# Kernel tuning notes

Measured on AMD Instinct MI355X. Metric: run time of the kernel, lower is better.

Reference implementation:

```python
import jax, jax.numpy as jnp
import numpy as np

N_NODES = 50000
N_EDGES = 800000
D_IN = 64
D_HID = 64
N_LAYERS = 3


def setup_inputs() -> dict:
    key = jax.random.key(0)
    ks = jax.random.split(key, 3 + 2 * N_LAYERS)
    x = jax.random.normal(ks[0], (N_NODES, D_IN), dtype=jnp.float32)
    edge_index = jax.random.randint(ks[1], (2, N_EDGES), 0, N_NODES, dtype=jnp.int64)
    edge_weight = jax.random.uniform(ks[2], (N_EDGES,), dtype=jnp.float32)
    inp = {"x": x, "edge_index": edge_index, "edge_weight": edge_weight}
    dims = [(D_IN, D_HID)] + [(D_HID, D_HID)] * (N_LAYERS - 1)
    for i, (din, dout) in enumerate(dims):
        # Glorot-style init like PyG GCNConv
        scale = jnp.sqrt(6.0 / (din + dout)).astype(jnp.float32)
        inp[f"W{i}"] = jax.random.uniform(ks[3 + 2 * i], (din, dout), dtype=jnp.float32, minval=-1.0, maxval=1.0) * scale
        inp[f"b{i}"] = jnp.zeros((dout,), dtype=jnp.float32)
    return inp


def _gcn_norm(edge_index, edge_weight, num_nodes, dtype):
    # Add self-loops with weight 1, then symmetric normalization (PyG gcn_norm).
    loop = jnp.arange(num_nodes)
    src = jnp.concatenate([edge_index[0], loop])
    dst = jnp.concatenate([edge_index[1], loop])
    w = jnp.concatenate([edge_weight, jnp.ones((num_nodes,), dtype=dtype)])
    deg = jax.ops.segment_sum(w, dst, num_segments=num_nodes)  # [N]
    dinv = jnp.where(deg > 0, jax.lax.rsqrt(deg), jnp.zeros_like(deg))
    norm = dinv[src] * w * dinv[dst]  # [E+N]
    return src, dst, norm


def reference(x, edge_index, edge_weight, W0, b0, W1, b1, W2, b2):
    N = x.shape[0]
    src, dst, norm = _gcn_norm(edge_index, edge_weight, N, x.dtype)
    for W, b in ((W0, b0), (W1, b1), (W2, b2)):
        h = x @ W                                   # [N, dout] linear first (PyG)
        msg = h[src] * norm[:, None]                # gather + scale per edge
        x = jax.ops.segment_sum(msg, dst, num_segments=N) + b  # scatter-add + bias
        x = jax.nn.relu(x)
    return x
```

## Files before the change

kernel.cpp:

```cpp
#include <hip/hip_runtime.h>

#define NN 50000
#define NE 800000
#define D  64
#define NB 782
#define NBLK 256
#define CHUNK 3125
#define CAP 1536
#define CAPTOT (NB * CAP)

__device__ __forceinline__ float blo(unsigned u) { return __uint_as_float(u << 16); }
__device__ __forceinline__ float bhi(unsigned u) { return __uint_as_float(u & 0xFFFF0000u); }
__device__ __forceinline__ unsigned short f2b(float f) {
    unsigned u = __float_as_uint(f);
    return (unsigned short)((u + 0x7FFFu + ((u >> 16) & 1u)) >> 16);
}

__global__ void k_init(int* __restrict__ cursor) {
    int i = blockIdx.x * blockDim.x + threadIdx.x;
    if (i < NB) cursor[i] = i * CAP;
}

__global__ __launch_bounds__(256) void p12(const int* __restrict__ src,
        const int* __restrict__ dst, const float* __restrict__ w,
        int* __restrict__ cursor, int2* __restrict__ stage) {
    __shared__ unsigned se[CHUNK];
    __shared__ float    sw[CHUNK];
    __shared__ int      lh[NB];
    int t = threadIdx.x;
    for (int i = t; i < NB; i += 256) lh[i] = 0;
    __syncthreads();
    int e0 = blockIdx.x * CHUNK;
    for (int i = t; i < CHUNK; i += 256) {
        int e = e0 + i;
        unsigned d = (unsigned)dst[e];
        unsigned s = (unsigned)src[e];
        float wv = w[e];
        unsigned pk = 0xFFFFFFFFu;
        if (d < NN) {
            pk = (s & 0xFFFFu) | ((d & 63u) << 16) | ((d >> 6) << 22);
            atomicAdd(&lh[d >> 6], 1);
        }
        se[i] = pk;
        sw[i] = wv;
    }
    __syncthreads();
    for (int i = t; i < NB; i += 256) {
        int c = lh[i];
        lh[i] = c ? atomicAdd(&cursor[i], c) : 0;
    }
    __syncthreads();
    for (int i = t; i < CHUNK; i += 256) {
        unsigned pk = se[i];
        if (pk != 0xFFFFFFFFu) {
            int bucket = (int)(pk >> 22);
            int pos = atomicAdd(&lh[bucket], 1);
            if (pos < (bucket + 1) * CAP)
                stage[pos] = make_int2((int)(pk & 0x3FFFFFu), __float_as_int(sw[i]));
        }
    }
}

__global__ __launch_bounds__(256) void p3_sort(const int2* __restrict__ stage,
        const int* __restrict__ cursor, int2* __restrict__ csr,
        int* __restrict__ row_ptr, int* __restrict__ row_deg, float* __restrict__ dinv) {
    __shared__ int   hist[64];
    __shared__ int   cur[64];
    __shared__ float wsum[64];
    int b = blockIdx.x, t = threadIdx.x;
    int g0 = b * CAP, g1 = cursor[b];
    if (t < 64) { hist[t] = 0; wsum[t] = 0.f; }
    __syncthreads();
    for (int j = g0 + t; j < g1; j += 256) {
        int2 pk = stage[j];
        int r = (pk.x >> 16) & 63;
        atomicAdd(&hist[r], 1);
        atomicAdd(&wsum[r], __int_as_float(pk.y));
    }
    __syncthreads();
    if (t == 0) {
        int s = g0;
        for (int r = 0; r < 64; ++r) { cur[r] = s; s += hist[r]; }
    }
    __syncthreads();
    if (t < 64) {
        int n = b * 64 + t;
        if (n < NN) {
            row_ptr[n] = cur[t];
            row_deg[n] = hist[t];
            dinv[n] = rsqrtf(wsum[t] + 1.0f);
        }
    }
    __syncthreads();
    for (int j = g0 + t; j < g1; j += 256) {
        int2 pk = stage[j];
        int r = (pk.x >> 16) & 63;
        int pos = atomicAdd(&cur[r], 1);
        csr[pos] = make_int2(pk.x & 0xFFFF, pk.y);
    }
}

__global__ __launch_bounds__(256) void gemm_pre_kernel(const float* __restrict__ x,
        const float* __restrict__ W, const float* __restrict__ dinv,
        unsigned short* __restrict__ hp) {
    __shared__ float xs[16][64];
    int t = threadIdx.x;
    int base = blockIdx.x * 16;
    for (int idx = t; idx < 16 * 64; idx += 256)
        xs[idx >> 6][idx & 63] = x[(size_t)(base + (idx >> 6)) * 64 + (idx & 63)];
    __syncthreads();
    int col = t & 63, rq = t >> 6;
    float wc[64];
#pragma unroll
    for (int k = 0; k < 64; ++k) wc[k] = W[k * 64 + col];
    float acc0 = 0.f, acc1 = 0.f, acc2 = 0.f, acc3 = 0.f;
#pragma unroll
    for (int k = 0; k < 64; ++k) {
        float wk = wc[k];
        acc0 += xs[rq     ][k] * wk;
        acc1 += xs[rq +  4][k] * wk;
        acc2 += xs[rq +  8][k] * wk;
        acc3 += xs[rq + 12][k] * wk;
    }
    int r = base + rq;
    hp[(size_t)(r     ) * 64 + col] = f2b(dinv[r     ] * acc0);
    hp[(size_t)(r +  4) * 64 + col] = f2b(dinv[r +  4] * acc1);
    hp[(size_t)(r +  8) * 64 + col] = f2b(dinv[r +  8] * acc2);
    hp[(size_t)(r + 12) * 64 + col] = f2b(dinv[r + 12] * acc3);
}

__device__ __forceinline__ float4 gather_row(int n, int fq,
        const int* __restrict__ row_ptr, const int* __restrict__ row_deg,
        const int2* __restrict__ csr, const uint2* __restrict__ hp64) {
    int s0 = row_ptr[n], s1 = s0 + row_deg[n];
    uint2 self = hp64[(size_t)n * 16 + fq];
    float ax = blo(self.x), ay = bhi(self.x), az = blo(self.y), aw = bhi(self.y);
    float bx = 0.f, by = 0.f, bz = 0.f, bw = 0.f;
    for (int base = s0; base < s1; base += 8) {
        uint2 u[8]; float wv[8];
#pragma unroll
        for (int jj = 0; jj < 8; ++jj) {
            int j = base + jj;
            if (j < s1) {
                int2 pk = csr[j];
                wv[jj] = __int_as_float(pk.y);
                u[jj]  = hp64[((size_t)(unsigned)pk.x << 4) + fq];
            } else {
                wv[jj] = 0.f;
                u[jj]  = make_uint2(0u, 0u);
            }
        }
#pragma unroll
        for (int jj = 0; jj < 8; jj += 2) {
            float w0 = wv[jj], w1 = wv[jj + 1];
            ax += w0 * blo(u[jj].x);     ay += w0 * bhi(u[jj].x);
            az += w0 * blo(u[jj].y);     aw += w0 * bhi(u[jj].y);
            bx += w1 * blo(u[jj + 1].x); by += w1 * bhi(u[jj + 1].x);
            bz += w1 * blo(u[jj + 1].y); bw += w1 * bhi(u[jj + 1].y);
        }
    }
    return make_float4(ax + bx, ay + by, az + bz, aw + bw);
}

__global__ __launch_bounds__(256) void fused_kernel(const int* __restrict__ row_ptr,
        const int* __restrict__ row_deg, const int2* __restrict__ csr,
        const float* __restrict__ dinv, const uint2* __restrict__ hp_cur,
        const float* __restrict__ bias, const float* __restrict__ Wn,
        unsigned short* __restrict__ hp_next) {
    __shared__ float ys[16][64];
    int t = threadIdx.x;
    int lane = t & 63, q = lane >> 4, fq = lane & 15;
    int ni = ((t >> 6) << 2) + q;
    int n = blockIdx.x * 16 + ni;
    float4 g = gather_row(n, fq, row_ptr, row_deg, csr, hp_cur);
    float dv = dinv[n];
    float4 bb = ((const float4*)bias)[fq];
    float4 y;
    y.x = fmaxf(dv * g.x + bb.x, 0.f);
    y.y = fmaxf(dv * g.y + bb.y, 0.f);
    y.z = fmaxf(dv * g.z + bb.z, 0.f);
    y.w = fmaxf(dv * g.w + bb.w, 0.f);
    ((float4*)ys[ni])[fq] = y;
    __syncthreads();
    int col = lane, rq = t >> 6;
    float wc[64];
#pragma unroll
    for (int k = 0; k < 64; ++k) wc[k] = Wn[k * 64 + col];
    float a0 = 0.f, a1 = 0.f, a2 = 0.f, a3 = 0.f;
#pragma unroll
    for (int k = 0; k < 64; ++k) {
        float wk = wc[k];
        a0 += ys[rq     ][k] * wk;
        a1 += ys[rq +  4][k] * wk;
        a2 += ys[rq +  8][k] * wk;
        a3 += ys[rq + 12][k] * wk;
    }
    int r = blockIdx.x * 16 + rq;
    hp_next[(size_t)(r     ) * 64 + col] = f2b(dinv[r     ] * a0);
    hp_next[(size_t)(r +  4) * 64 + col] = f2b(dinv[r +  4] * a1);
    hp_next[(size_t)(r +  8) * 64 + col] = f2b(dinv[r +  8] * a2);
    hp_next[(size_t)(r + 12) * 64 + col] = f2b(dinv[r + 12] * a3);
}

__global__ __launch_bounds__(256) void final_kernel(const int* __restrict__ row_ptr,
        const int* __restrict__ row_deg, const int2* __restrict__ csr,
        const float* __restrict__ dinv, const uint2* __restrict__ hp_cur,
        const float* __restrict__ bias, float* __restrict__ out) {
    int t = threadIdx.x;
    int lane = t & 63, q = lane >> 4, fq = lane & 15;
    int n = blockIdx.x * 16 + ((t >> 6) << 2) + q;
    float4 g = gather_row(n, fq, row_ptr, row_deg, csr, hp_cur);
    float dv = dinv[n];
    float4 bb = ((const float4*)bias)[fq];
    float4 r;
    r.x = fmaxf(dv * g.x + bb.x, 0.f);
    r.y = fmaxf(dv * g.y + bb.y, 0.f);
    r.z = fmaxf(dv * g.z + bb.z, 0.f);
    r.w = fmaxf(dv * g.w + bb.w, 0.f);
    ((float4*)out)[(size_t)n * 16 + fq] = r;
}

extern "C" void kernel_launch(void* const* d_in, const int* in_sizes, int n_in,
                              void* d_out, int out_size, void* d_ws, size_t ws_size,
                              hipStream_t stream) {
    const float* x  = (const float*)d_in[0];
    const int*   ei = (const int*)d_in[1];
    const float* ew = (const float*)d_in[2];
    const float* W0 = (const float*)d_in[3];
    const float* b0 = (const float*)d_in[4];
    const float* W1 = (const float*)d_in[5];
    const float* b1 = (const float*)d_in[6];
    const float* W2 = (const float*)d_in[7];
    const float* b2 = (const float*)d_in[8];
    float*       out = (float*)d_out;

    const int* src = ei;
    const int* dst = ei + NE;

    int2*  stage   = (int2*)d_ws;
    int2*  csr     = stage + CAPTOT;
    int*   cursor  = (int*)(csr + CAPTOT);
    int*   row_ptr = cursor + NB;
    int*   row_deg = row_ptr + NN;
    float* dinv    = (float*)(row_deg + NN);
    unsigned short* hpA = (unsigned short*)(dinv + NN);
    unsigned short* hpB = hpA + (size_t)NN * 64;

    k_init<<<1, 1024, 0, stream>>>(cursor);
    p12<<<NBLK, 256, 0, stream>>>(src, dst, ew, cursor, stage);
    p3_sort<<<NB, 256, 0, stream>>>(stage, cursor, csr, row_ptr, row_deg, dinv);

    gemm_pre_kernel<<<NN / 16, 256, 0, stream>>>(x, W0, dinv, hpA);
    fused_kernel<<<NN / 16, 256, 0, stream>>>(row_ptr, row_deg, csr, dinv,
            (const uint2*)hpA, b0, W1, hpB);
    fused_kernel<<<NN / 16, 256, 0, stream>>>(row_ptr, row_deg, csr, dinv,
            (const uint2*)hpB, b1, W2, hpA);
    final_kernel<<<NN / 16, 256, 0, stream>>>(row_ptr, row_deg, csr, dinv,
            (const uint2*)hpA, b2, out);
}
```

Measured before the change: 218.7 us.

## Gather each node with a full wave splitting edges across lanes

The aggregation now assigns one 64-lane wave per node instead of 16 lanes per node. The lanes form 8 edge slots of 8 lanes, and each lane loads 16 bytes of bf16 features. Partial sums are combined with cross-lane xor shuffles, and blocks grow to 1024 threads so that 16 nodes still fit per block. This targets imbalance and serialized latency on high-degree rows and raises memory-level parallelism per edge. The cost is four times as many threads, shuffle reductions, and a dense step where each lane now computes one output rather than four. The hp buffers are also moved earlier in the workspace, likely for alignment of the 16-byte loads.

```diff
diff --git a/kernel.cpp b/kernel.cpp
--- a/kernel.cpp
+++ b/kernel.cpp
@@ -129,95 +129,106 @@
     hp[(size_t)(r + 12) * 64 + col] = f2b(dinv[r + 12] * acc3);
 }
 
-__device__ __forceinline__ float4 gather_row(int n, int fq,
+__device__ __forceinline__ void gather_wave(int n, int slot, int fo,
         const int* __restrict__ row_ptr, const int* __restrict__ row_deg,
-        const int2* __restrict__ csr, const uint2* __restrict__ hp64) {
+        const int2* __restrict__ csr, const uint4* __restrict__ hp4,
+        float acc[8]) {
     int s0 = row_ptr[n], s1 = s0 + row_deg[n];
-    uint2 self = hp64[(size_t)n * 16 + fq];
-    float ax = blo(self.x), ay = bhi(self.x), az = blo(self.y), aw = bhi(self.y);
-    float bx = 0.f, by = 0.f, bz = 0.f, bw = 0.f;
-    for (int base = s0; base < s1; base += 8) {
-        uint2 u[8]; float wv[8];
-#pragma unroll
-        for (int jj = 0; jj < 8; ++jj) {
-            int j = base + jj;
-            if (j < s1) {
-                int2 pk = csr[j];
-                wv[jj] = __int_as_float(pk.y);
-                u[jj]  = hp64[((size_t)(unsigned)pk.x << 4) + fq];
-            } else {
-                wv[jj] = 0.f;
-                u[jj]  = make_uint2(0u, 0u);
-            }
-        }
-#pragma unroll
-        for (int jj = 0; jj < 8; jj += 2) {
-            float w0 = wv[jj], w1 = wv[jj + 1];
-            ax += w0 * blo(u[jj].x);     ay += w0 * bhi(u[jj].x);
-            az += w0 * blo(u[jj].y);     aw += w0 * bhi(u[jj].y);
-            bx += w1 * blo(u[jj + 1].x); by += w1 * bhi(u[jj + 1].x);
-            bz += w1 * blo(u[jj + 1].y); bw += w1 * bhi(u[jj + 1].y);
-        }
-    }
-    return make_float4(ax + bx, ay + by, az + bz, aw + bw);
-}
-
-__global__ __launch_bounds__(256) void fused_kernel(const int* __restrict__ row_ptr,
+    uint4 sv = hp4[(size_t)n * 8 + fo];
+    bool keep = (slot == 0);
+    acc[0] = keep ? blo(sv.x) : 0.f;  acc[1] = keep ? bhi(sv.x) : 0.f;
+    acc[2] = keep ? blo(sv.y) : 0.f;  acc[3] = keep ? bhi(sv.y) : 0.f;
+    acc[4] = keep ? blo(sv.z) : 0.f;  acc[5] = keep ? bhi(sv.z) : 0.f;
+    acc[6] = keep ? blo(sv.w) : 0.f;  acc[7] = keep ? bhi(sv.w) : 0.f;
+    for (int base = s0; base < s1; base += 16) {
+        int j0 = base + slot, j1 = base + 8 + slot;
+        int src0 = 0; float w0 = 0.f;
+        int src1 = 0; float w1 = 0.f;
+        if (j0 < s1) { int2 pk = csr[j0]; src0 = pk.x; w0 = __int_as_float(pk.y); }
+        if (j1 < s1) { int2 pk = csr[j1]; src1 = pk.x; w1 = __int_as_float(pk.y); }
+        uint4 u0 = hp4[(size_t)src0 * 8 + fo];
+        uint4 u1 = hp4[(size_t)src1 * 8 + fo];
+        acc[0] += w0 * blo(u0.x);  acc[1] += w0 * bhi(u0.x);
+        acc[2] += w0 * blo(u0.y);  acc[3] += w0 * bhi(u0.y);
+        acc[4] += w0 * blo(u0.z);  acc[5] += w0 * bhi(u0.z);
+        acc[6] += w0 * blo(u0.w);  acc[7] += w0 * bhi(u0.w);
+        acc[0] += w1 * blo(u1.x);  acc[1] += w1 * bhi(u1.x);
+        acc[2] += w1 * blo(u1.y);  acc[3] += w1 * bhi(u1.y);
+        acc[4] += w1 * blo(u1.z);  acc[5] += w1 * bhi(u1.z);
+        acc[6] += w1 * blo(u1.w);  acc[7] += w1 * bhi(u1.w);
+    }
+#pragma unroll
+    for (int m = 8; m <= 32; m <<= 1) {
+#pragma unroll
+        for (int i = 0; i < 8; ++i) acc[i] += __shfl_xor(acc[i], m, 64);
+    }
+}
+
+__global__ __launch_bounds__(1024) void fused_kernel(const int* __restrict__ row_ptr,
         const int* __restrict__ row_deg, const int2* __restrict__ csr,
-        const float* __restrict__ dinv, const uint2* __restrict__ hp_cur,
+        const float* __restrict__ dinv, const uint4* __restrict__ hp_cur,
         const float* __restrict__ bias, const float* __restrict__ Wn,
         unsigned short* __restrict__ hp_next) {
     __shared__ float ys[16][64];
     int t = threadIdx.x;
-    int lane = t & 63, q = lane >> 4, fq = lane & 15;
-    int ni = ((t >> 6) << 2) + q;
-    int n = blockIdx.x * 16 + ni;
-    float4 g = gather_row(n, fq, row_ptr, row_deg, csr, hp_cur);
-    float dv = dinv[n];
-    float4 bb = ((const float4*)bias)[fq];
-    float4 y;
-    y.x = fmaxf(dv * g.x + bb.x, 0.f);
-    y.y = fmaxf(dv * g.y + bb.y, 0.f);
-    y.z = fmaxf(dv * g.z + bb.z, 0.f);
-    y.w = fmaxf(dv * g.w + bb.w, 0.f);
-    ((float4*)ys[ni])[fq] = y;
-    __syncthreads();
-    int col = lane, rq = t >> 6;
+    int wid = t >> 6, lane = t & 63, slot = lane >> 3, fo = lane & 7;
+    int n = blockIdx.x * 16 + wid;
+    float acc[8];
+    gather_wave(n, slot, fo, row_ptr, row_deg, csr, hp_cur, acc);
+    if (slot == 0) {
+        float dv = dinv[n];
+        float4 b0v = ((const float4*)bias)[fo * 2];
+        float4 b1v = ((const float4*)bias)[fo * 2 + 1];
+        float4 y0, y1;
+        y0.x = fmaxf(dv * acc[0] + b0v.x, 0.f);
+        y0.y = fmaxf(dv * acc[1] + b0v.y, 0.f);
+        y0.z = fmaxf(dv * acc[2] + b0v.z, 0.f);
+        y0.w = fmaxf(dv * acc[3] + b0v.w, 0.f);
+        y1.x = fmaxf(dv * acc[4] + b1v.x, 0.f);
+        y1.y = fmaxf(dv * acc[5] + b1v.y, 0.f);
+        y1.z = fmaxf(dv * acc[6] + b1v.z, 0.f);
+        y1.w = fmaxf(dv * acc[7] + b1v.w, 0.f);
+        ((float4*)&ys[wid][fo * 8])[0] = y0;
+        ((float4*)&ys[wid][fo * 8])[1] = y1;
+    }
+    __syncthreads();
+    int col = lane, rq = wid;
     float wc[64];
 #pragma unroll
     for (int k = 0; k < 64; ++k) wc[k] = Wn[k * 64 + col];
-    float a0 = 0.f, a1 = 0.f, a2 = 0.f, a3 = 0.f;
-#pragma unroll
-    for (int k = 0; k < 64; ++k) {
-        float wk = wc[k];
-        a0 += ys[rq     ][k] * wk;
-        a1 += ys[rq +  4][k] * wk;
-        a2 += ys[rq +  8][k] * wk;
-        a3 += ys[rq + 12][k] * wk;
-    }
+    float a = 0.f;
+#pragma unroll
+    for (int k = 0; k < 64; ++k) a += ys[rq][k] * wc[k];
     int r = blockIdx.x * 16 + rq;
-    hp_next[(size_t)(r     ) * 64 + col] = f2b(dinv[r     ] * a0);
-    hp_next[(size_t)(r +  4) * 64 + col] = f2b(dinv[r +  4] * a1);
-    hp_next[(size_t)(r +  8) * 64 + col] = f2b(dinv[r +  8] * a2);
-    hp_next[(size_t)(r + 12) * 64 + col] = f2b(dinv[r + 12] * a3);
-}
-
-__global__ __launch_bounds__(256) void final_kernel(const int* __restrict__ row_ptr,
+    hp_next[(size_t)r * 64 + col] = f2b(dinv[r] * a);
+}
+
+__global__ __launch_bounds__(1024) void final_kernel(const int* __restrict__ row_ptr,
         const int* __restrict__ row_deg, const int2* __restrict__ csr,
-        const float* __restrict__ dinv, const uint2* __restrict__ hp_cur,
+        const float* __restrict__ dinv, const uint4* __restrict__ hp_cur,
         const float* __restrict__ bias, float* __restrict__ out) {
     int t = threadIdx.x;
-    int lane = t & 63, q = lane >> 4, fq = lane & 15;
-    int n = blockIdx.x * 16 + ((t >> 6) << 2) + q;
-    float4 g = gather_row(n, fq, row_ptr, row_deg, csr, hp_cur);
-    float dv = dinv[n];
-    float4 bb = ((const float4*)bias)[fq];
-    float4 r;
-    r.x = fmaxf(dv * g.x + bb.x, 0.f);
-    r.y = fmaxf(dv * g.y + bb.y, 0.f);
-    r.z = fmaxf(dv * g.z + bb.z, 0.f);
-    r.w = fmaxf(dv * g.w + bb.w, 0.f);
-    ((float4*)out)[(size_t)n * 16 + fq] = r;
+    int wid = t >> 6, lane = t & 63, slot = lane >> 3, fo = lane & 7;
+    int n = blockIdx.x * 16 + wid;
+    float acc[8];
+    gather_wave(n, slot, fo, row_ptr, row_deg, csr, hp_cur, acc);
+    if (slot == 0) {
+        float dv = dinv[n];
+        float4 b0v = ((const float4*)bias)[fo * 2];
+        float4 b1v = ((const float4*)bias)[fo * 2 + 1];
+        float4 r0, r1;
+        r0.x = fmaxf(dv * acc[0] + b0v.x, 0.f);
+        r0.y = fmaxf(dv * acc[1] + b0v.y, 0.f);
+        r0.z = fmaxf(dv * acc[2] + b0v.z, 0.f);
+        r0.w = fmaxf(dv * acc[3] + b0v.w, 0.f);
+        r1.x = fmaxf(dv * acc[4] + b1v.x, 0.f);
+        r1.y = fmaxf(dv * acc[5] + b1v.y, 0.f);
+        r1.z = fmaxf(dv * acc[6] + b1v.z, 0.f);
+        r1.w = fmaxf(dv * acc[7] + b1v.w, 0.f);
+        float4* orow = (float4*)(out + (size_t)n * 64 + fo * 8);
+        orow[0] = r0;
+        orow[1] = r1;
+    }
 }
 
 extern "C" void kernel_launch(void* const* d_in, const int* in_sizes, int n_in,
@@ -239,22 +250,22 @@
 
     int2*  stage   = (int2*)d_ws;
     int2*  csr     = stage + CAPTOT;
-    int*   cursor  = (int*)(csr + CAPTOT);
+    unsigned short* hpA = (unsigned short*)(csr + CAPTOT);
+    unsigned short* hpB = hpA + (size_t)NN * 64;
+    int*   cursor  = (int*)(hpB + (size_t)NN * 64);
     int*   row_ptr = cursor + NB;
     int*   row_deg = row_ptr + NN;
     float* dinv    = (float*)(row_deg + NN);
-    unsigned short* hpA = (unsigned short*)(dinv + NN);
-    unsigned short* hpB = hpA + (size_t)NN * 64;
 
     k_init<<<1, 1024, 0, stream>>>(cursor);
     p12<<<NBLK, 256, 0, stream>>>(src, dst, ew, cursor, stage);
     p3_sort<<<NB, 256, 0, stream>>>(stage, cursor, csr, row_ptr, row_deg, dinv);
 
     gemm_pre_kernel<<<NN / 16, 256, 0, stream>>>(x, W0, dinv, hpA);
-    fused_kernel<<<NN / 16, 256, 0, stream>>>(row_ptr, row_deg, csr, dinv,
-            (const uint2*)hpA, b0, W1, hpB);
-    fused_kernel<<<NN / 16, 256, 0, stream>>>(row_ptr, row_deg, csr, dinv,
-            (const uint2*)hpB, b1, W2, hpA);
-    final_kernel<<<NN / 16, 256, 0, stream>>>(row_ptr, row_deg, csr, dinv,
-            (const uint2*)hpA, b2, out);
-}
+    fused_kernel<<<NN / 16, 1024, 0, stream>>>(row_ptr, row_deg, csr, dinv,
+            (const uint4*)hpA, b0, W1, hpB);
+    fused_kernel<<<NN / 16, 1024, 0, stream>>>(row_ptr, row_deg, csr, dinv,
+            (const uint4*)hpB, b1, W2, hpA);
+    final_kernel<<<NN / 16, 1024, 0, stream>>>(row_ptr, row_deg, csr, dinv,
+            (const uint4*)hpA, b2, out);
+}
```

Result: slower. 272.2 us (+24.5%).
